# Kernel optimization log

Measured on AMD Instinct MI355X. Metric: run time of the kernel, lower is better.

## Reference

```python
import jax, jax.numpy as jnp
import numpy as np

HIDDEN = 1024
NEG_INF = jnp.float32(-1e7)


def setup_inputs() -> dict:
    key = jax.random.key(0)
    ks = jax.random.split(key, 9)
    B, S, H = 4, 2048, HIDDEN
    std = 1.0 / np.sqrt(H)
    return {
        "queries": jax.random.normal(ks[0], (B, S, H), jnp.float32),
        "keys": jax.random.normal(ks[1], (B, S, H), jnp.float32),
        "values": jax.random.normal(ks[2], (B, S, H), jnp.float32),
        "Wq": jax.random.uniform(ks[3], (H, H), jnp.float32, -std, std),
        "bq": jax.random.uniform(ks[4], (H,), jnp.float32, -std, std),
        "Wk": jax.random.uniform(ks[5], (H, H), jnp.float32, -std, std),
        "bk": jax.random.uniform(ks[6], (H,), jnp.float32, -std, std),
        "Wv": jax.random.uniform(ks[7], (H, H), jnp.float32, -std, std),
        "bv": jax.random.uniform(ks[8], (H,), jnp.float32, -std, std),
    }


def reference(queries, keys, values, Wq, bq, Wk, bk, Wv, bv):
    # q,k,v: (B, S, H) linear projections (torch Linear: x @ W.T + b)
    q = jnp.einsum('bth,oh->bto', queries, Wq) + bq
    k = jnp.einsum('bsh,oh->bso', keys, Wk) + bk
    v = jnp.einsum('bsh,oh->bso', values, Wv) + bv
    scale = jax.lax.rsqrt(jnp.float32(q.shape[-1] * 0 + Wq.shape[0]))
    # scores[b, s, t] = <k_s, q_t> * scale   (key index s, query index t)
    scores = jnp.einsum('bsh,bth->bst', k, q) * scale
    S, T = scores.shape[1], scores.shape[2]
    # torch.tril(ones * -1e7, diagonal=-1): add -1e7 where s > t (strictly lower)
    mask = jnp.where(jnp.arange(S)[:, None] > jnp.arange(T)[None, :], NEG_INF, 0.0)
    attn = jax.nn.softmax(scores + mask, axis=1)  # softmax over key dim (dim=1)
    context = jnp.einsum('bst,bsh->bth', attn, v)  # (B, T, H)
    return context, attn
```

## Files before the change

### kernel.cpp

```cpp
#include <hip/hip_runtime.h>
#include <math.h>

typedef __bf16 bf16x8 __attribute__((ext_vector_type(8)));
typedef __bf16 bf16x4 __attribute__((ext_vector_type(4)));
typedef float f32x4 __attribute__((ext_vector_type(4)));

#define HD 1024
#define SEQ 2048
#define NB 4
#define WEL (HD * HD)

__device__ inline bf16x8 load8cvt(const __bf16* p) { return *(const bf16x8*)p; }
__device__ inline bf16x8 load8cvt(const float* p) {
    f32x4 a = *(const f32x4*)p;
    f32x4 b = *(const f32x4*)(p + 4);
    bf16x8 r;
#pragma unroll
    for (int i = 0; i < 4; ++i) { r[i] = (__bf16)a[i]; r[i + 4] = (__bf16)b[i]; }
    return r;
}

__device__ inline f32x4 load4f(const float* p) { return *(const f32x4*)p; }
__device__ inline f32x4 load4f(const __bf16* p) {
    bf16x4 v = *(const bf16x4*)p;
    f32x4 r;
#pragma unroll
    for (int i = 0; i < 4; ++i) r[i] = (float)v[i];
    return r;
}

__device__ inline void gld_lds16(const void* g, void* l) {
    __builtin_amdgcn_global_load_lds(
        (const __attribute__((address_space(1))) unsigned int*)g,
        (__attribute__((address_space(3))) unsigned int*)l, 16, 0, 0);
}

template <typename T>
__device__ inline void stage_tile(const T* __restrict__ G, int ld, __bf16* s, int tid)
{
    const int r  = tid >> 3;
    const int co = (tid & 7) * 8;
    if constexpr (sizeof(T) == 2) {
        __bf16* dst = s + (tid >> 6) * 512;
#pragma unroll
        for (int c = 0; c < 4; ++c)
            gld_lds16(G + (long)(c * 32 + r) * ld + co, dst + c * 2048);
    } else {
#pragma unroll
        for (int c = 0; c < 4; ++c)
            *(bf16x8*)(s + c * 2048 + tid * 8) = load8cvt(G + (long)(c * 32 + r) * ld + co);
    }
}

struct Proj3 {
    const void* A[3];
    const void* W[3];
    const float* bias[3];
    __bf16* C[3];
    int vtmask;
};

template <typename TA, typename TW>
__global__ __launch_bounds__(256) void gemm_proj(Proj3 p)
{
    __shared__ __bf16 sA[128 * 64];
    __shared__ __bf16 sB[128 * 64];

    const int tid = threadIdx.x;
    const int z  = blockIdx.z;
    const int n0 = blockIdx.x * 128;
    const int m0 = blockIdx.y * 128;
    const bool vt = (p.vtmask >> z) & 1;

    const TA* Ag = (const TA*)p.A[z] + (long)m0 * HD;
    const TW* Wg = (const TW*)p.W[z] + (long)n0 * HD;
    const float* bias = p.bias[z];
    __bf16* C = p.C[z];

    const int lane = tid & 63;
    const int l15  = lane & 15;
    const int quad = lane >> 4;
    const int wave = tid >> 6;
    const int wm = (wave >> 1) * 64;
    const int wn = (wave & 1) * 64;

    f32x4 acc[4][4];
    const f32x4 zero = {0.f, 0.f, 0.f, 0.f};
#pragma unroll
    for (int i = 0; i < 4; ++i)
#pragma unroll
        for (int j = 0; j < 4; ++j) acc[i][j] = zero;

    for (int kc = 0; kc < HD; kc += 64) {
        stage_tile(Ag + kc, HD, sA, tid);
        stage_tile(Wg + kc, HD, sB, tid);
        __syncthreads();
#pragma unroll
        for (int kk = 0; kk < 64; kk += 32) {
            bf16x8 af[4], bf[4];
#pragma unroll
            for (int i = 0; i < 4; ++i)
                af[i] = *(const bf16x8*)&sA[(wm + i * 16 + l15) * 64 + quad * 8 + kk];
#pragma unroll
            for (int j = 0; j < 4; ++j)
                bf[j] = *(const bf16x8*)&sB[(wn + j * 16 + l15) * 64 + quad * 8 + kk];
#pragma unroll
            for (int i = 0; i < 4; ++i)
#pragma unroll
                for (int j = 0; j < 4; ++j)
                    acc[i][j] = __builtin_amdgcn_mfma_f32_16x16x32_bf16(af[i], bf[j], acc[i][j], 0, 0, 0);
        }
        __syncthreads();
    }

#pragma unroll
    for (int j = 0; j < 4; ++j) {
        const int col = n0 + wn + j * 16 + l15;
        const float bv = bias[col];
#pragma unroll
        for (int i = 0; i < 4; ++i) {
#pragma unroll
            for (int r = 0; r < 4; ++r) {
                const int row = m0 + wm + i * 16 + quad * 4 + r;
                const float v = acc[i][j][r] + bv;
                if (vt) {
                    C[(((long)(row >> 11) * HD) + col) * SEQ + (row & (SEQ - 1))] = (__bf16)v;
                } else {
                    C[(long)row * HD + col] = (__bf16)v;
                }
            }
        }
    }
}

template <bool TRI, bool CKLIM, bool EXPSUM, typename OutT>
__global__ __launch_bounds__(256) void gemm_bt(
    const __bf16* __restrict__ A, long strideA, int lda,
    const __bf16* __restrict__ B, long strideB, int ldb,
    OutT* __restrict__ C, long strideC, int ldc,
    float* __restrict__ gsum,
    int K, float alpha)
{
    __shared__ __bf16 sA[128 * 64];
    __shared__ __bf16 sB[128 * 64];
    __shared__ float csum[128];

    const int tid = threadIdx.x;
    int n0, m0;
    if (TRI) {
        const int L = blockIdx.x;
        int tb = (int)((sqrtf(8.f * L + 1.f) - 1.f) * 0.5f);
        while ((tb + 1) * (tb + 2) / 2 <= L) ++tb;
        while (tb * (tb + 1) / 2 > L) --tb;
        const int sb = L - tb * (tb + 1) / 2;
        n0 = tb * 128;
        m0 = sb * 128;
    } else {
        n0 = blockIdx.x * 128;
        m0 = blockIdx.y * 128;
    }

    const __bf16* Ag = A + (long)blockIdx.z * strideA + (long)m0 * lda;
    const __bf16* Bg = B + (long)blockIdx.z * strideB + (long)n0 * ldb;
    C += (long)blockIdx.z * strideC;
    if (EXPSUM) {
        gsum += (long)blockIdx.z * SEQ;
        if (tid < 128) csum[tid] = 0.f;
    }

    const int lane = tid & 63;
    const int l15  = lane & 15;
    const int quad = lane >> 4;
    const int wave = tid >> 6;
    const int wm = (wave >> 1) * 64;
    const int wn = (wave & 1) * 64;

    f32x4 acc[4][4];
    const f32x4 zero = {0.f, 0.f, 0.f, 0.f};
#pragma unroll
    for (int i = 0; i < 4; ++i)
#pragma unroll
        for (int j = 0; j < 4; ++j) acc[i][j] = zero;

    const int Kend = CKLIM ? min(K, m0 + 128) : K;

    for (int kc = 0; kc < Kend; kc += 64) {
        stage_tile(Ag + kc, lda, sA, tid);
        stage_tile(Bg + kc, ldb, sB, tid);
        __syncthreads();
#pragma unroll
        for (int kk = 0; kk < 64; kk += 32) {
            bf16x8 af[4], bf[4];
#pragma unroll
            for (int i = 0; i < 4; ++i)
                af[i] = *(const bf16x8*)&sA[(wm + i * 16 + l15) * 64 + quad * 8 + kk];
#pragma unroll
            for (int j = 0; j < 4; ++j)
                bf[j] = *(const bf16x8*)&sB[(wn + j * 16 + l15) * 64 + quad * 8 + kk];
#pragma unroll
            for (int i = 0; i < 4; ++i)
#pragma unroll
                for (int j = 0; j < 4; ++j)
                    acc[i][j] = __builtin_amdgcn_mfma_f32_16x16x32_bf16(af[i], bf[j], acc[i][j], 0, 0, 0);
        }
        __syncthreads();
    }

#pragma unroll
    for (int j = 0; j < 4; ++j) {
        const int col = n0 + wn + j * 16 + l15;
        float part = 0.f;
#pragma unroll
        for (int i = 0; i < 4; ++i) {
#pragma unroll
            for (int r = 0; r < 4; ++r) {
                const int row = m0 + wm + i * 16 + quad * 4 + r;
                float v = acc[i][j][r] * alpha;
                if (EXPSUM) {
                    v = __expf(v);
                    if (row <= col) part += v;
                }
                C[(long)row * ldc + col] = (OutT)v;
            }
        }
        if (EXPSUM) atomicAdd(&csum[wn + j * 16 + l15], part);
    }
    if (EXPSUM) {
        __syncthreads();
        if (tid < 128) atomicAdd(&gsum[n0 + tid], csum[tid]);
    }
}

template <typename ET>
__global__ __launch_bounds__(256) void scale_emit(
    const ET* __restrict__ E, float* __restrict__ Out,
    const float* __restrict__ csum, __bf16* __restrict__ AT)
{
    __shared__ __bf16 tile[64][65];
    const int b = blockIdx.z;
    const int t0 = blockIdx.x * 128;
    const int s0 = blockIdx.y * 128;
    const ET* Eb = E + (long)b * SEQ * SEQ;
    float* Ob = Out + (long)b * SEQ * SEQ;
    __bf16* Ab = AT + (long)b * SEQ * SEQ;
    const int tid = threadIdx.x;

    if (s0 > t0 + 127) {
        const f32x4 z4 = {0.f, 0.f, 0.f, 0.f};
        const int c4 = (tid & 31) * 4;
        for (int r = tid >> 5; r < 128; r += 8)
            *(f32x4*)&Ob[(long)(s0 + r) * SEQ + t0 + c4] = z4;
        return;
    }

#pragma unroll
    for (int ds = 0; ds < 2; ++ds) {
#pragma unroll
        for (int dt = 0; dt < 2; ++dt) {
            const int ss = s0 + ds * 64, tt = t0 + dt * 64;
            const int c4 = (tid & 15) * 4;
            const int tcol = tt + c4;
            const f32x4 sv = *(const f32x4*)&csum[(long)b * SEQ + tcol];
            f32x4 inv;
#pragma unroll
            for (int k = 0; k < 4; ++k) inv[k] = 1.0f / sv[k];
#pragma unroll
            for (int r0 = 0; r0 < 64; r0 += 16) {
                const int s = ss + r0 + (tid >> 4);
                f32x4 e = load4f(&Eb[(long)s * SEQ + tcol]);
                f32x4 p;
#pragma unroll
                for (int k = 0; k < 4; ++k)
                    p[k] = (s <= tcol + k) ? e[k] * inv[k] : 0.f;
                *(f32x4*)&Ob[(long)s * SEQ + tcol] = p;
#pragma unroll
                for (int k = 0; k < 4; ++k)
                    tile[r0 + (tid >> 4)][c4 + k] = (__bf16)p[k];
            }
            __syncthreads();
            const int tr = tid >> 2;
            const int sc = (tid & 3) * 16;
            __bf16 v[16];
#pragma unroll
            for (int jj = 0; jj < 16; ++jj) v[jj] = tile[sc + jj][tr];
            *(bf16x8*)&Ab[(long)(tt + tr) * SEQ + ss + sc]     = *(bf16x8*)v;
            *(bf16x8*)&Ab[(long)(tt + tr) * SEQ + ss + sc + 8] = *(bf16x8*)(v + 8);
            __syncthreads();
        }
    }
}

struct CvtJob { const float* in; __bf16* out; int nblk; };
struct Cvt6 { CvtJob j[6]; };
__global__ __launch_bounds__(256) void cvt_bf16(Cvt6 c)
{
    const CvtJob jb = c.j[blockIdx.y];
    if ((int)blockIdx.x >= jb.nblk) return;
    const long i = ((long)blockIdx.x * 256 + threadIdx.x) * 8;
    *(bf16x8*)&jb.out[i] = load8cvt(&jb.in[i]);
}

extern "C" void kernel_launch(void* const* d_in, const int* in_sizes, int n_in,
                              void* d_out, int out_size, void* d_ws, size_t ws_size,
                              hipStream_t stream)
{
    const float* queries = (const float*)d_in[0];
    const float* keys    = (const float*)d_in[1];
    const float* values  = (const float*)d_in[2];
    const float* Wq = (const float*)d_in[3];
    const float* bq = (const float*)d_in[4];
    const float* Wk = (const float*)d_in[5];
    const float* bk = (const float*)d_in[6];
    const float* Wv = (const float*)d_in[7];
    const float* bv = (const float*)d_in[8];

    const long tokens = (long)NB * SEQ;
    const long pe = tokens * HD;
    const size_t SLOT = (size_t)pe * sizeof(__bf16);
    const int ABLK = (int)(pe / 2048);
    const int WBLK = WEL / 2048;

    float* outCtx  = (float*)d_out;
    float* outAttn = outCtx + tokens * HD;
    float* colsum = outCtx;
    __bf16* wb = (__bf16*)outAttn;
    __bf16* Wqb = wb, *Wkb = wb + WEL, *Wvb = wb + 2 * WEL;

    const dim3 blk(256);
    hipMemsetAsync(colsum, 0, (size_t)NB * SEQ * sizeof(float), stream);

    char* w = (char*)d_ws;
    __bf16 *qp, *kp, *vT, *attnT;
    const dim3 gProj(HD / 128, tokens / 128, 3);

    bool ebig = false;
    __bf16* Ebf = nullptr;

    if (ws_size >= 6 * SLOT) {
        __bf16* xq = (__bf16*)w;
        __bf16* xk = (__bf16*)(w + SLOT);
        __bf16* xv = (__bf16*)(w + 2 * SLOT);
        qp = (__bf16*)(w + 3 * SLOT);
        kp = (__bf16*)(w + 4 * SLOT);
        vT = (__bf16*)(w + 5 * SLOT);
        Ebf = (__bf16*)w;
        attnT = (__bf16*)(w + 2 * SLOT);
        ebig = true;

        Cvt6 cv = {{{queries, xq, ABLK}, {keys, xk, ABLK}, {values, xv, ABLK},
                    {Wq, Wqb, WBLK}, {Wk, Wkb, WBLK}, {Wv, Wvb, WBLK}}};
        cvt_bf16<<<dim3(ABLK, 6), blk, 0, stream>>>(cv);
        Proj3 pj = {{xq, xk, xv}, {Wqb, Wkb, Wvb}, {bq, bk, bv}, {qp, kp, vT}, 4};
        gemm_proj<__bf16, __bf16><<<gProj, blk, 0, stream>>>(pj);
    } else if (ws_size >= 4 * SLOT) {
        __bf16* x0 = (__bf16*)w;
        qp = (__bf16*)(w + SLOT);
        kp = (__bf16*)(w + 2 * SLOT);
        __bf16* x1 = (__bf16*)(w + 3 * SLOT);
        vT = x1;
        attnT = (__bf16*)d_ws;

        Cvt6 cv = {{{queries, x0, ABLK}, {keys, x1, ABLK},
                    {Wq, Wqb, WBLK}, {Wk, Wkb, WBLK}, {Wv, Wvb, WBLK},
                    {nullptr, nullptr, 0}}};
        cvt_bf16<<<dim3(ABLK, 5), blk, 0, stream>>>(cv);
        Proj3 pqk = {{x0, x1, nullptr}, {Wqb, Wkb, nullptr}, {bq, bk, nullptr},
                     {qp, kp, nullptr}, 0};
        gemm_proj<__bf16, __bf16><<<dim3(HD / 128, tokens / 128, 2), blk, 0, stream>>>(pqk);
        Cvt6 cvv = {{{values, x0, ABLK}, {nullptr, nullptr, 0}, {nullptr, nullptr, 0},
                     {nullptr, nullptr, 0}, {nullptr, nullptr, 0}, {nullptr, nullptr, 0}}};
        cvt_bf16<<<dim3(ABLK, 1), blk, 0, stream>>>(cvv);
        Proj3 pv = {{x0, nullptr, nullptr}, {Wvb, nullptr, nullptr},
                    {bv, nullptr, nullptr}, {vT, nullptr, nullptr}, 1};
        gemm_proj<__bf16, __bf16><<<dim3(HD / 128, tokens / 128, 1), blk, 0, stream>>>(pv);
    } else {
        qp = (__bf16*)w;
        kp = (__bf16*)(w + SLOT);
        vT = (__bf16*)(w + 2 * SLOT);
        attnT = (__bf16*)d_ws;
        Proj3 pj = {{queries, keys, values}, {Wq, Wk, Wv}, {bq, bk, bv},
                    {qp, kp, vT}, 4};
        gemm_proj<float, float><<<gProj, blk, 0, stream>>>(pj);
    }

    if (ebig) {
        gemm_bt<true, false, true, __bf16><<<dim3(136, 1, NB), blk, 0, stream>>>(
            kp, (long)SEQ * HD, HD, qp, (long)SEQ * HD, HD,
            Ebf, (long)SEQ * SEQ, SEQ, colsum, HD, 0.03125f);
        scale_emit<__bf16><<<dim3(SEQ / 128, SEQ / 128, NB), blk, 0, stream>>>(
            Ebf, outAttn, colsum, attnT);
    } else {
        gemm_bt<true, false, true, float><<<dim3(136, 1, NB), blk, 0, stream>>>(
            kp, (long)SEQ * HD, HD, qp, (long)SEQ * HD, HD,
            outAttn, (long)SEQ * SEQ, SEQ, colsum, HD, 0.03125f);
        scale_emit<float><<<dim3(SEQ / 128, SEQ / 128, NB), blk, 0, stream>>>(
            outAttn, outAttn, colsum, attnT);
    }

    gemm_bt<false, true, false, float><<<dim3(HD / 128, SEQ / 128, NB), blk, 0, stream>>>(
        attnT, (long)SEQ * SEQ, SEQ, vT, (long)HD * SEQ, SEQ,
        outCtx, (long)SEQ * HD, HD, nullptr, SEQ, 1.0f);
}
```

Baseline: 401.3 us.

## XOR-swizzle LDS tiles and remap blocks for XCD-local L2 reuse

Staging now XOR-swizzles the 16-byte column chunk of each LDS row by the row index, and fragment reads apply the same swizzle. This is meant to remove bank conflicts on the MFMA operand reads. All GEMM launches also change to a 1D grid whose block index is remapped with (L&7)*per + (L>>3), so consecutive tiles land on the same XCD and share L2. The remap assumes the grid size is divisible by 8 and hardcodes the tile counts.

```diff
diff --git a/kernel.cpp b/kernel.cpp
--- a/kernel.cpp
+++ b/kernel.cpp
@@ -39,7 +39,7 @@
 __device__ inline void stage_tile(const T* __restrict__ G, int ld, __bf16* s, int tid)
 {
     const int r  = tid >> 3;
-    const int co = (tid & 7) * 8;
+    const int co = ((tid & 7) ^ (r & 7)) * 8;
     if constexpr (sizeof(T) == 2) {
         __bf16* dst = s + (tid >> 6) * 512;
 #pragma unroll
@@ -50,6 +50,11 @@
         for (int c = 0; c < 4; ++c)
             *(bf16x8*)(s + c * 2048 + tid * 8) = load8cvt(G + (long)(c * 32 + r) * ld + co);
     }
+}
+
+__device__ inline bf16x8 frag_read(const __bf16* s, int row, int c)
+{
+    return *(const bf16x8*)&s[row * 64 + ((c ^ (row & 7)) * 8)];
 }
 
 struct Proj3 {
@@ -67,9 +72,12 @@
     __shared__ __bf16 sB[128 * 64];
 
     const int tid = threadIdx.x;
-    const int z  = blockIdx.z;
-    const int n0 = blockIdx.x * 128;
-    const int m0 = blockIdx.y * 128;
+    const int L = blockIdx.x;
+    const int per = gridDim.x >> 3;
+    const int wrk = (L & 7) * per + (L >> 3);
+    const int n0 = (wrk & 7) * 128;
+    const int m0 = ((wrk >> 3) & 63) * 128;
+    const int z  = wrk >> 9;
     const bool vt = (p.vtmask >> z) & 1;
 
     const TA* Ag = (const TA*)p.A[z] + (long)m0 * HD;
@@ -97,13 +105,14 @@
         __syncthreads();
 #pragma unroll
         for (int kk = 0; kk < 64; kk += 32) {
+            const int c8 = quad + (kk >> 3);
             bf16x8 af[4], bf[4];
 #pragma unroll
             for (int i = 0; i < 4; ++i)
-                af[i] = *(const bf16x8*)&sA[(wm + i * 16 + l15) * 64 + quad * 8 + kk];
+                af[i] = frag_read(sA, wm + i * 16 + l15, c8);
 #pragma unroll
             for (int j = 0; j < 4; ++j)
-                bf[j] = *(const bf16x8*)&sB[(wn + j * 16 + l15) * 64 + quad * 8 + kk];
+                bf[j] = frag_read(sB, wn + j * 16 + l15, c8);
 #pragma unroll
             for (int i = 0; i < 4; ++i)
 #pragma unroll
@@ -146,25 +155,30 @@
     __shared__ float csum[128];
 
     const int tid = threadIdx.x;
-    int n0, m0;
+    const int L = blockIdx.x;
+    const int per = gridDim.x >> 3;
+    const int wrk = (L & 7) * per + (L >> 3);
+    int n0, m0, z;
     if (TRI) {
-        const int L = blockIdx.x;
-        int tb = (int)((sqrtf(8.f * L + 1.f) - 1.f) * 0.5f);
-        while ((tb + 1) * (tb + 2) / 2 <= L) ++tb;
-        while (tb * (tb + 1) / 2 > L) --tb;
-        const int sb = L - tb * (tb + 1) / 2;
+        const int Lt = wrk % 136;
+        z = wrk / 136;
+        int tb = (int)((sqrtf(8.f * Lt + 1.f) - 1.f) * 0.5f);
+        while ((tb + 1) * (tb + 2) / 2 <= Lt) ++tb;
+        while (tb * (tb + 1) / 2 > Lt) --tb;
+        const int sb = Lt - tb * (tb + 1) / 2;
         n0 = tb * 128;
         m0 = sb * 128;
     } else {
-        n0 = blockIdx.x * 128;
-        m0 = blockIdx.y * 128;
-    }
-
-    const __bf16* Ag = A + (long)blockIdx.z * strideA + (long)m0 * lda;
-    const __bf16* Bg = B + (long)blockIdx.z * strideB + (long)n0 * ldb;
-    C += (long)blockIdx.z * strideC;
+        n0 = (wrk & 7) * 128;
+        m0 = ((wrk >> 3) & 15) * 128;
+        z  = wrk >> 7;
+    }
+
+    const __bf16* Ag = A + (long)z * strideA + (long)m0 * lda;
+    const __bf16* Bg = B + (long)z * strideB + (long)n0 * ldb;
+    C += (long)z * strideC;
     if (EXPSUM) {
-        gsum += (long)blockIdx.z * SEQ;
+        gsum += (long)z * SEQ;
         if (tid < 128) csum[tid] = 0.f;
     }
 
@@ -190,13 +204,14 @@
         __syncthreads();
 #pragma unroll
         for (int kk = 0; kk < 64; kk += 32) {
+            const int c8 = quad + (kk >> 3);
             bf16x8 af[4], bf[4];
 #pragma unroll
             for (int i = 0; i < 4; ++i)
-                af[i] = *(const bf16x8*)&sA[(wm + i * 16 + l15) * 64 + quad * 8 + kk];
+                af[i] = frag_read(sA, wm + i * 16 + l15, c8);
 #pragma unroll
             for (int j = 0; j < 4; ++j)
-                bf[j] = *(const bf16x8*)&sB[(wn + j * 16 + l15) * 64 + quad * 8 + kk];
+                bf[j] = frag_read(sB, wn + j * 16 + l15, c8);
 #pragma unroll
             for (int i = 0; i < 4; ++i)
 #pragma unroll
@@ -331,7 +346,6 @@
 
     char* w = (char*)d_ws;
     __bf16 *qp, *kp, *vT, *attnT;
-    const dim3 gProj(HD / 128, tokens / 128, 3);
 
     bool ebig = false;
     __bf16* Ebf = nullptr;
@@ -351,7 +365,7 @@
                     {Wq, Wqb, WBLK}, {Wk, Wkb, WBLK}, {Wv, Wvb, WBLK}}};
         cvt_bf16<<<dim3(ABLK, 6), blk, 0, stream>>>(cv);
         Proj3 pj = {{xq, xk, xv}, {Wqb, Wkb, Wvb}, {bq, bk, bv}, {qp, kp, vT}, 4};
-        gemm_proj<__bf16, __bf16><<<gProj, blk, 0, stream>>>(pj);
+        gemm_proj<__bf16, __bf16><<<dim3(512 * 3), blk, 0, stream>>>(pj);
     } else if (ws_size >= 4 * SLOT) {
         __bf16* x0 = (__bf16*)w;
         qp = (__bf16*)(w + SLOT);
@@ -366,13 +380,13 @@
         cvt_bf16<<<dim3(ABLK, 5), blk, 0, stream>>>(cv);
         Proj3 pqk = {{x0, x1, nullptr}, {Wqb, Wkb, nullptr}, {bq, bk, nullptr},
                      {qp, kp, nullptr}, 0};
-        gemm_proj<__bf16, __bf16><<<dim3(HD / 128, tokens / 128, 2), blk, 0, stream>>>(pqk);
+        gemm_proj<__bf16, __bf16><<<dim3(512 * 2), blk, 0, stream>>>(pqk);
         Cvt6 cvv = {{{values, x0, ABLK}, {nullptr, nullptr, 0}, {nullptr, nullptr, 0},
                      {nullptr, nullptr, 0}, {nullptr, nullptr, 0}, {nullptr, nullptr, 0}}};
         cvt_bf16<<<dim3(ABLK, 1), blk, 0, stream>>>(cvv);
         Proj3 pv = {{x0, nullptr, nullptr}, {Wvb, nullptr, nullptr},
                     {bv, nullptr, nullptr}, {vT, nullptr, nullptr}, 1};
-        gemm_proj<__bf16, __bf16><<<dim3(HD / 128, tokens / 128, 1), blk, 0, stream>>>(pv);
+        gemm_proj<__bf16, __bf16><<<dim3(512), blk, 0, stream>>>(pv);
     } else {
         qp = (__bf16*)w;
         kp = (__bf16*)(w + SLOT);
@@ -380,24 +394,24 @@
         attnT = (__bf16*)d_ws;
         Proj3 pj = {{queries, keys, values}, {Wq, Wk, Wv}, {bq, bk, bv},
                     {qp, kp, vT}, 4};
-        gemm_proj<float, float><<<gProj, blk, 0, stream>>>(pj);
+        gemm_proj<float, float><<<dim3(512 * 3), blk, 0, stream>>>(pj);
     }
 
     if (ebig) {
-        gemm_bt<true, false, true, __bf16><<<dim3(136, 1, NB), blk, 0, stream>>>(
+        gemm_bt<true, false, true, __bf16><<<dim3(544), blk, 0, stream>>>(
             kp, (long)SEQ * HD, HD, qp, (long)SEQ * HD, HD,
             Ebf, (long)SEQ * SEQ, SEQ, colsum, HD, 0.03125f);
         scale_emit<__bf16><<<dim3(SEQ / 128, SEQ / 128, NB), blk, 0, stream>>>(
             Ebf, outAttn, colsum, attnT);
     } else {
-        gemm_bt<true, false, true, float><<<dim3(136, 1, NB), blk, 0, stream>>>(
+        gemm_bt<true, false, true, float><<<dim3(544), blk, 0, stream>>>(
             kp, (long)SEQ * HD, HD, qp, (long)SEQ * HD, HD,
             outAttn, (long)SEQ * SEQ, SEQ, colsum, HD, 0.03125f);
         scale_emit<float><<<dim3(SEQ / 128, SEQ / 128, NB), blk, 0, stream>>>(
             outAttn, outAttn, colsum, attnT);
     }
 
-    gemm_bt<false, true, false, float><<<dim3(HD / 128, SEQ / 128, NB), blk, 0, stream>>>(
+    gemm_bt<false, true, false, float><<<dim3(512), blk, 0, stream>>>(
         attnT, (long)SEQ * SEQ, SEQ, vT, (long)HD * SEQ, SEQ,
         outCtx, (long)SEQ * HD, HD, nullptr, SEQ, 1.0f);
 }
```

After: 388.3 us. -3.2%, faster.
